# Kernel tuning notes

Measured on AMD Instinct MI355X. Metric: run time of the kernel, lower is better.

The kernel has to match this reference:

```python
import jax, jax.numpy as jnp
import numpy as np

BATCH = 2048
FID_NUM = 65536
AVG_ACTIVE = 20.0  # ~active fids per example


def setup_inputs() -> dict:
    key = jax.random.key(0)
    k1, k2, k3 = jax.random.split(key, 3)
    # binary one-hot gate, ~AVG_ACTIVE ones per row (matches _get_model_feed_dict)
    gate = (jax.random.uniform(k1, (BATCH, FID_NUM)) < (AVG_ACTIVE / FID_NUM)).astype(jnp.float32)
    sparse_bias = 0.01 * jax.random.normal(k2, (FID_NUM,), dtype=jnp.float32)
    global_bias = jnp.zeros((1,), dtype=jnp.float32)
    label = (jax.random.uniform(k3, (BATCH,)) < 0.5).astype(jnp.float32)
    return {"bias_fid_gate": gate, "sparse_bias": sparse_bias,
            "global_bias": global_bias, "label": label}


def reference(bias_fid_gate, sparse_bias, global_bias, label):
    # bias_input = gate * bias; logits = reduce_sum(bias_input, axis=1) + global_bias
    logits = jnp.sum(bias_fid_gate * sparse_bias, axis=1) + global_bias[0]  # [B]
    pred = jax.nn.sigmoid(logits)
    # tf.nn.sigmoid_cross_entropy_with_logits, then reduce_sum
    per_ex = jnp.maximum(logits, 0.0) - logits * label + jnp.log1p(jnp.exp(-jnp.abs(logits)))
    loss = jnp.sum(per_ex)
    return logits, pred, loss
```

## Files before the change

kernel.cpp:

```cpp
#include <hip/hip_runtime.h>
#include <math.h>

#define BATCH 2048
#define FID 65536
#define NT 256
#define ROWS 4
#define NV (FID / 4)
#define KSPLIT 4
#define NVH (NV / KSPLIT)

typedef float vf4 __attribute__((ext_vector_type(4)));

__global__ __launch_bounds__(NT, 8) void lr_partial(
        const float* __restrict__ gate,
        const float* __restrict__ bias,
        float* __restrict__ out) {
    const int kb = blockIdx.x & (KSPLIT - 1);
    const int rb = blockIdx.x >> 2;
    const int r0 = rb * ROWS;
    const vf4* __restrict__ b4 = (const vf4*)bias;
    const vf4* __restrict__ g4 = (const vf4*)gate + (size_t)r0 * NV;
    const int i0 = kb * NVH;
    const int i1 = i0 + NVH;

    float a0 = 0.f, a1 = 0.f, a2 = 0.f, a3 = 0.f;

    #pragma unroll 2
    for (int i = i0 + threadIdx.x; i < i1; i += NT) {
        vf4 v  = b4[i];
        vf4 g0 = __builtin_nontemporal_load(&g4[i]);
        vf4 g1 = __builtin_nontemporal_load(&g4[i + NV]);
        vf4 g2 = __builtin_nontemporal_load(&g4[i + 2 * NV]);
        vf4 g3 = __builtin_nontemporal_load(&g4[i + 3 * NV]);
        a0 = fmaf(g0.x, v.x, a0); a0 = fmaf(g0.y, v.y, a0);
        a0 = fmaf(g0.z, v.z, a0); a0 = fmaf(g0.w, v.w, a0);
        a1 = fmaf(g1.x, v.x, a1); a1 = fmaf(g1.y, v.y, a1);
        a1 = fmaf(g1.z, v.z, a1); a1 = fmaf(g1.w, v.w, a1);
        a2 = fmaf(g2.x, v.x, a2); a2 = fmaf(g2.y, v.y, a2);
        a2 = fmaf(g2.z, v.z, a2); a2 = fmaf(g2.w, v.w, a2);
        a3 = fmaf(g3.x, v.x, a3); a3 = fmaf(g3.y, v.y, a3);
        a3 = fmaf(g3.z, v.z, a3); a3 = fmaf(g3.w, v.w, a3);
    }

    #pragma unroll
    for (int off = 32; off > 0; off >>= 1) {
        a0 += __shfl_down(a0, off, 64);
        a1 += __shfl_down(a1, off, 64);
        a2 += __shfl_down(a2, off, 64);
        a3 += __shfl_down(a3, off, 64);
    }

    __shared__ float wsum[NT / 64][ROWS];
    const int wave = threadIdx.x >> 6;
    const int lane = threadIdx.x & 63;
    if (lane == 0) {
        wsum[wave][0] = a0; wsum[wave][1] = a1;
        wsum[wave][2] = a2; wsum[wave][3] = a3;
    }
    __syncthreads();

    if (threadIdx.x < ROWS) {
        const int r = threadIdx.x;
        float s = wsum[0][r] + wsum[1][r] + wsum[2][r] + wsum[3][r];
        atomicAdd(&out[r0 + r], s);
    }
}

__global__ __launch_bounds__(NT) void lr_finish(
        const float* __restrict__ gbias,
        const float* __restrict__ label,
        float* __restrict__ out) {
    const float gb = gbias[0];
    float acc = 0.0f;
    for (int i = threadIdx.x; i < BATCH; i += NT) {
        float x = out[i] + gb;
        float l = label[i];
        out[i] = x;
        out[BATCH + i] = 1.0f / (1.0f + expf(-x));
        acc += fmaxf(x, 0.0f) - x * l + log1pf(expf(-fabsf(x)));
    }
    #pragma unroll
    for (int off = 32; off > 0; off >>= 1)
        acc += __shfl_down(acc, off, 64);

    __shared__ float wsum[NT / 64];
    const int wave = threadIdx.x >> 6;
    const int lane = threadIdx.x & 63;
    if (lane == 0) wsum[wave] = acc;
    __syncthreads();
    if (threadIdx.x == 0)
        out[2 * BATCH] = wsum[0] + wsum[1] + wsum[2] + wsum[3];
}

extern "C" void kernel_launch(void* const* d_in, const int* in_sizes, int n_in,
                              void* d_out, int out_size, void* d_ws, size_t ws_size,
                              hipStream_t stream) {
    const float* gate  = (const float*)d_in[0];
    const float* bias  = (const float*)d_in[1];
    const float* gbias = (const float*)d_in[2];
    const float* label = (const float*)d_in[3];
    float* out = (float*)d_out;

    hipMemsetAsync(out, 0, BATCH * sizeof(float), stream);

    lr_partial<<<(BATCH / ROWS) * KSPLIT, NT, 0, stream>>>(gate, bias, out);
    lr_finish<<<1, NT, 0, stream>>>(gbias, label, out);
}
```

Before: 658.6 us.

## Use one block per row and drop split-K atomics and memset

Restructures the GEMV so each block reduces one full gate row instead of four rows over a quarter of the feature range. The per-row result is written directly, so the memset launch and the atomicAdd accumulation are no longer needed. The trade-off is that the bias vector is now read once per row rather than once per four rows, which adds L2 traffic, and the grid shrinks to 2048 blocks that each do more work.

```diff
diff --git a/kernel.cpp b/kernel.cpp
--- a/kernel.cpp
+++ b/kernel.cpp
@@ -4,66 +4,40 @@
 #define BATCH 2048
 #define FID 65536
 #define NT 256
-#define ROWS 4
 #define NV (FID / 4)
-#define KSPLIT 4
-#define NVH (NV / KSPLIT)
 
 typedef float vf4 __attribute__((ext_vector_type(4)));
 
-__global__ __launch_bounds__(NT, 8) void lr_partial(
+__global__ __launch_bounds__(NT, 8) void lr_row(
         const float* __restrict__ gate,
         const float* __restrict__ bias,
         float* __restrict__ out) {
-    const int kb = blockIdx.x & (KSPLIT - 1);
-    const int rb = blockIdx.x >> 2;
-    const int r0 = rb * ROWS;
+    const int r = blockIdx.x;
     const vf4* __restrict__ b4 = (const vf4*)bias;
-    const vf4* __restrict__ g4 = (const vf4*)gate + (size_t)r0 * NV;
-    const int i0 = kb * NVH;
-    const int i1 = i0 + NVH;
+    const vf4* __restrict__ g4 = (const vf4*)gate + (size_t)r * NV;
 
-    float a0 = 0.f, a1 = 0.f, a2 = 0.f, a3 = 0.f;
-
-    #pragma unroll 2
-    for (int i = i0 + threadIdx.x; i < i1; i += NT) {
-        vf4 v  = b4[i];
-        vf4 g0 = __builtin_nontemporal_load(&g4[i]);
-        vf4 g1 = __builtin_nontemporal_load(&g4[i + NV]);
-        vf4 g2 = __builtin_nontemporal_load(&g4[i + 2 * NV]);
-        vf4 g3 = __builtin_nontemporal_load(&g4[i + 3 * NV]);
-        a0 = fmaf(g0.x, v.x, a0); a0 = fmaf(g0.y, v.y, a0);
-        a0 = fmaf(g0.z, v.z, a0); a0 = fmaf(g0.w, v.w, a0);
-        a1 = fmaf(g1.x, v.x, a1); a1 = fmaf(g1.y, v.y, a1);
-        a1 = fmaf(g1.z, v.z, a1); a1 = fmaf(g1.w, v.w, a1);
-        a2 = fmaf(g2.x, v.x, a2); a2 = fmaf(g2.y, v.y, a2);
-        a2 = fmaf(g2.z, v.z, a2); a2 = fmaf(g2.w, v.w, a2);
-        a3 = fmaf(g3.x, v.x, a3); a3 = fmaf(g3.y, v.y, a3);
-        a3 = fmaf(g3.z, v.z, a3); a3 = fmaf(g3.w, v.w, a3);
+    float a = 0.f;
+    #pragma unroll 4
+    for (int i = threadIdx.x; i < NV; i += NT) {
+        vf4 v = b4[i];
+        vf4 g = __builtin_nontemporal_load(&g4[i]);
+        a = fmaf(g.x, v.x, a);
+        a = fmaf(g.y, v.y, a);
+        a = fmaf(g.z, v.z, a);
+        a = fmaf(g.w, v.w, a);
     }
 
     #pragma unroll
-    for (int off = 32; off > 0; off >>= 1) {
-        a0 += __shfl_down(a0, off, 64);
-        a1 += __shfl_down(a1, off, 64);
-        a2 += __shfl_down(a2, off, 64);
-        a3 += __shfl_down(a3, off, 64);
-    }
+    for (int off = 32; off > 0; off >>= 1)
+        a += __shfl_down(a, off, 64);
 
-    __shared__ float wsum[NT / 64][ROWS];
+    __shared__ float wsum[NT / 64];
     const int wave = threadIdx.x >> 6;
     const int lane = threadIdx.x & 63;
-    if (lane == 0) {
-        wsum[wave][0] = a0; wsum[wave][1] = a1;
-        wsum[wave][2] = a2; wsum[wave][3] = a3;
-    }
+    if (lane == 0) wsum[wave] = a;
     __syncthreads();
-
-    if (threadIdx.x < ROWS) {
-        const int r = threadIdx.x;
-        float s = wsum[0][r] + wsum[1][r] + wsum[2][r] + wsum[3][r];
-        atomicAdd(&out[r0 + r], s);
-    }
+    if (threadIdx.x == 0)
+        out[r] = wsum[0] + wsum[1] + wsum[2] + wsum[3];
 }
 
 __global__ __launch_bounds__(NT) void lr_finish(
@@ -101,8 +75,6 @@
     const float* label = (const float*)d_in[3];
     float* out = (float*)d_out;
 
-    hipMemsetAsync(out, 0, BATCH * sizeof(float), stream);
-
-    lr_partial<<<(BATCH / ROWS) * KSPLIT, NT, 0, stream>>>(gate, bias, out);
+    lr_row<<<BATCH, NT, 0, stream>>>(gate, bias, out);
     lr_finish<<<1, NT, 0, stream>>>(gbias, label, out);
 }
```

After: 654.5 us. About the same (-0.6%).
